# Performance work log

Hardware: AMD Instinct MI355X
Metric: run time of the kernel (lower is better)

## Reference

```python
import jax, jax.numpy as jnp
import numpy as np

NUM_GRAPHS = 4096
EPS = 1e-6

def _ln(x, g, b):
    mu = jnp.mean(x, axis=-1, keepdims=True)
    var = jnp.mean(jnp.square(x - mu), axis=-1, keepdims=True)
    return (x - mu) * jax.lax.rsqrt(var + EPS) * g + b

def setup_inputs() -> dict:
    key = jax.random.key(0)
    ks = jax.random.split(key, 8)
    N, D, H, DRUG = 262144, 128, 8, 128
    feat = jax.random.normal(ks[0], (N, D), dtype=jnp.float32)
    batch = jnp.sort(jax.random.randint(ks[1], (N,), 0, NUM_GRAPHS)).astype(jnp.int64)
    def lin(k, fi, fo):
        lim = 1.0 / np.sqrt(fi)
        return jax.random.uniform(k, (fi, fo), jnp.float32, -lim, lim)
    return {
        'feat': feat, 'batch': batch,
        'W1': lin(ks[2], D, 64), 'b1': jnp.zeros((64,), jnp.float32),
        'g1': jnp.ones((64,), jnp.float32), 'beta1': jnp.zeros((64,), jnp.float32),
        'W2': lin(ks[3], 64, H), 'b2': jnp.zeros((H,), jnp.float32),
        'W3': lin(ks[4], H * D, D), 'b3': jnp.zeros((D,), jnp.float32),
        'g3': jnp.ones((D,), jnp.float32), 'beta3': jnp.zeros((D,), jnp.float32),
        'W4': lin(ks[5], D, DRUG), 'b4': jnp.zeros((DRUG,), jnp.float32),
        'g4': jnp.ones((DRUG,), jnp.float32), 'beta4': jnp.zeros((DRUG,), jnp.float32),
    }

def reference(feat, batch, W1, b1, g1, beta1, W2, b2, W3, b3, g3, beta3, W4, b4, g4, beta4):
    seg = batch.astype(jnp.int32)
    # ATFC: Linear -> LeakyReLU -> LayerNorm -> Linear
    h = jax.nn.leaky_relu(feat @ W1 + b1)
    h = _ln(h, g1, beta1)
    att = jnp.exp(h @ W2 + b2)                      # [N, H]
    # segment softmax normalization
    s = jax.ops.segment_sum(att, seg, num_segments=NUM_GRAPHS)  # [B, H]
    att = att / s[seg]
    # weighted aggregation: outer product + segment sum -> [B, H, D]
    out = jax.ops.segment_sum(att[:, :, None] * feat[:, None, :], seg, num_segments=NUM_GRAPHS)
    out = out.reshape(NUM_GRAPHS, -1)               # [B, H*D]
    # output block (dropout is identity in eval mode)
    o = _ln(jax.nn.leaky_relu(out @ W3 + b3), g3, beta3)
    o = _ln(jax.nn.leaky_relu(o @ W4 + b4), g4, beta4)
    return o
```

## Files before the change

kernel.cpp:

```cpp
#include <hip/hip_runtime.h>
#include <math.h>

#define NG 4096
#define NN 262144
#define D 128
#define M1 64
#define NH 8
#define EPS 1e-6f

typedef __attribute__((ext_vector_type(8))) short short8;
typedef __attribute__((ext_vector_type(4))) float f32x4;

__device__ inline float leaky(float x) { return x > 0.f ? x : 0.01f * x; }

__device__ inline short f2bf(float f) {
  union { float f; unsigned u; } v; v.f = f;
  unsigned r = (v.u + 0x7fffu + ((v.u >> 16) & 1u)) >> 16;
  return (short)r;
}

__global__ void k0_offs(const int* __restrict__ batch, int* __restrict__ offs) {
  int i = blockIdx.x * 256 + threadIdx.x;
  if (i <= NG) {
    int lo = 0, hi = NN;
    while (lo < hi) {
      int mid = (lo + hi) >> 1;
      if (batch[mid] < i) lo = mid + 1; else hi = mid;
    }
    offs[i] = lo;
  }
}

__global__ __launch_bounds__(256) void k1_att(
    const float* __restrict__ feat, const float* __restrict__ W1,
    const float* __restrict__ b1, const float* __restrict__ g1,
    const float* __restrict__ beta1, const float* __restrict__ W2,
    const float* __restrict__ b2, float* __restrict__ att) {
  __shared__ short W1T[M1][D + 8];
  __shared__ short W2T[16][M1 + 8];
  __shared__ short hb[128][72];

  int t = threadIdx.x;
#pragma unroll
  for (int i = 0; i < 8; ++i) {
    int idx4 = t + 256 * i;
    int k = idx4 >> 4;
    int j = (idx4 & 15) * 4;
    float4 wv = *(const float4*)(W1 + k * M1 + j);
    W1T[j + 0][k] = f2bf(wv.x);
    W1T[j + 1][k] = f2bf(wv.y);
    W1T[j + 2][k] = f2bf(wv.z);
    W1T[j + 3][k] = f2bf(wv.w);
  }
#pragma unroll
  for (int i = 0; i < 4; ++i) {
    int e = t * 4 + i;
    int hh = e >> 6, j = e & 63;
    W2T[hh][j] = (hh < NH) ? f2bf(W2[j * NH + hh]) : (short)0;
  }
  __syncthreads();

  int w = t >> 6, l = t & 63;
  int lr = l & 15, lq = l >> 4;
  int nb = blockIdx.x * 128 + w * 32;

  short8 afr[2][4];
#pragma unroll
  for (int mt = 0; mt < 2; ++mt) {
    const float* rp = feat + (size_t)(nb + mt * 16 + lr) * D + lq * 8;
#pragma unroll
    for (int c = 0; c < 4; ++c) {
      float4 x0 = *(const float4*)(rp + c * 32);
      float4 x1 = *(const float4*)(rp + c * 32 + 4);
      short8 a;
      a[0] = f2bf(x0.x); a[1] = f2bf(x0.y); a[2] = f2bf(x0.z); a[3] = f2bf(x0.w);
      a[4] = f2bf(x1.x); a[5] = f2bf(x1.y); a[6] = f2bf(x1.z); a[7] = f2bf(x1.w);
      afr[mt][c] = a;
    }
  }

  f32x4 acc[2][4];
#pragma unroll
  for (int mt = 0; mt < 2; ++mt)
#pragma unroll
    for (int nt = 0; nt < 4; ++nt) acc[mt][nt] = (f32x4){0.f, 0.f, 0.f, 0.f};
#pragma unroll
  for (int c = 0; c < 4; ++c) {
#pragma unroll
    for (int nt = 0; nt < 4; ++nt) {
      short8 bfr = *(const short8*)&W1T[nt * 16 + lr][c * 32 + lq * 8];
      acc[0][nt] = __builtin_amdgcn_mfma_f32_16x16x32_bf16(afr[0][c], bfr, acc[0][nt], 0, 0, 0);
      acc[1][nt] = __builtin_amdgcn_mfma_f32_16x16x32_bf16(afr[1][c], bfr, acc[1][nt], 0, 0, 0);
    }
  }

  float b1v[4], g1v[4], btv[4];
#pragma unroll
  for (int nt = 0; nt < 4; ++nt) {
    b1v[nt] = b1[nt * 16 + lr];
    g1v[nt] = g1[nt * 16 + lr];
    btv[nt] = beta1[nt * 16 + lr];
  }
#pragma unroll
  for (int mt = 0; mt < 2; ++mt) {
#pragma unroll
    for (int r = 0; r < 4; ++r) {
      float x[4], s1 = 0.f, s2 = 0.f;
#pragma unroll
      for (int nt = 0; nt < 4; ++nt) {
        float xv = leaky(acc[mt][nt][r] + b1v[nt]);
        x[nt] = xv;
        s1 += xv;
        s2 = fmaf(xv, xv, s2);
      }
#pragma unroll
      for (int off = 1; off < 16; off <<= 1) {
        s1 += __shfl_xor(s1, off);
        s2 += __shfl_xor(s2, off);
      }
      float mu = s1 * (1.f / M1);
      float var = s2 * (1.f / M1) - mu * mu;
      float inv = rsqrtf(var + EPS);
      int node = w * 32 + mt * 16 + lq * 4 + r;
#pragma unroll
      for (int nt = 0; nt < 4; ++nt)
        hb[node][nt * 16 + lr] = f2bf((x[nt] - mu) * inv * g1v[nt] + btv[nt]);
    }
  }
  __syncthreads();

  f32x4 acc2[2];
  acc2[0] = (f32x4){0.f, 0.f, 0.f, 0.f};
  acc2[1] = (f32x4){0.f, 0.f, 0.f, 0.f};
#pragma unroll
  for (int c2 = 0; c2 < 2; ++c2) {
    short8 bfr2 = *(const short8*)&W2T[lr][c2 * 32 + lq * 8];
#pragma unroll
    for (int mt = 0; mt < 2; ++mt) {
      short8 af2 = *(const short8*)&hb[w * 32 + mt * 16 + lr][c2 * 32 + lq * 8];
      acc2[mt] = __builtin_amdgcn_mfma_f32_16x16x32_bf16(af2, bfr2, acc2[mt], 0, 0, 0);
    }
  }
  if (lr < NH) {
    float b2v = b2[lr];
#pragma unroll
    for (int mt = 0; mt < 2; ++mt)
#pragma unroll
      for (int r = 0; r < 4; ++r) {
        int node = nb + mt * 16 + lq * 4 + r;
        att[(size_t)node * NH + lr] = expf(acc2[mt][r] + b2v);
      }
  }
}

__global__ __launch_bounds__(256) void k2_agg(
    const float* __restrict__ feat, const int* __restrict__ offs,
    const float* __restrict__ att, float* __restrict__ out_row) {
  __shared__ float4 red[4][NH][32];
  __shared__ float reds[4][NH][32];

  int g = blockIdx.x, t = threadIdx.x;
  int d4 = t & 31, sub = t >> 5;
  int lo = offs[g], hi = offs[g + 1];

  float4 acc[NH];
  float sa[NH];
#pragma unroll
  for (int h = 0; h < NH; ++h) {
    acc[h] = make_float4(0.f, 0.f, 0.f, 0.f);
    sa[h] = 0.f;
  }

  const float4* fv = (const float4*)feat;
  const float4* av = (const float4*)att;
  int n = lo + sub;
  float4 fc, a0c, a1c;
  if (n < hi) {
    fc = fv[(size_t)n * 32 + d4];
    a0c = av[(size_t)n * 2];
    a1c = av[(size_t)n * 2 + 1];
  }
  while (n < hi) {
    int n2 = n + 8;
    float4 fn, a0n, a1n;
    if (n2 < hi) {
      fn = fv[(size_t)n2 * 32 + d4];
      a0n = av[(size_t)n2 * 2];
      a1n = av[(size_t)n2 * 2 + 1];
    }
    float ah[NH] = {a0c.x, a0c.y, a0c.z, a0c.w, a1c.x, a1c.y, a1c.z, a1c.w};
#pragma unroll
    for (int h = 0; h < NH; ++h) {
      acc[h].x = fmaf(ah[h], fc.x, acc[h].x);
      acc[h].y = fmaf(ah[h], fc.y, acc[h].y);
      acc[h].z = fmaf(ah[h], fc.z, acc[h].z);
      acc[h].w = fmaf(ah[h], fc.w, acc[h].w);
      sa[h] += ah[h];
    }
    fc = fn; a0c = a0n; a1c = a1n;
    n = n2;
  }

  if (sub >= 4) {
#pragma unroll
    for (int h = 0; h < NH; ++h) {
      red[sub - 4][h][d4] = acc[h];
      reds[sub - 4][h][d4] = sa[h];
    }
  }
  __syncthreads();
  if (sub < 4) {
#pragma unroll
    for (int h = 0; h < NH; ++h) {
      float4 r = red[sub][h][d4];
      acc[h].x += r.x; acc[h].y += r.y; acc[h].z += r.z; acc[h].w += r.w;
      sa[h] += reds[sub][h][d4];
    }
  }
  __syncthreads();
  if (sub >= 2 && sub < 4) {
#pragma unroll
    for (int h = 0; h < NH; ++h) {
      red[sub - 2][h][d4] = acc[h];
      reds[sub - 2][h][d4] = sa[h];
    }
  }
  __syncthreads();
  if (sub < 2) {
#pragma unroll
    for (int h = 0; h < NH; ++h) {
      float4 r = red[sub][h][d4];
      acc[h].x += r.x; acc[h].y += r.y; acc[h].z += r.z; acc[h].w += r.w;
      sa[h] += reds[sub][h][d4];
    }
  }
  __syncthreads();
  if (sub == 1) {
#pragma unroll
    for (int h = 0; h < NH; ++h) {
      red[0][h][d4] = acc[h];
      reds[0][h][d4] = sa[h];
    }
  }
  __syncthreads();
  if (sub == 0) {
    float4* orow = (float4*)(out_row + (size_t)g * (NH * D));
#pragma unroll
    for (int h = 0; h < NH; ++h) {
      float4 r = red[0][h][d4];
      float st = sa[h] + reds[0][h][d4];
      float inv = st > 0.f ? 1.f / st : 0.f;
      float4 v;
      v.x = (acc[h].x + r.x) * inv;
      v.y = (acc[h].y + r.y) * inv;
      v.z = (acc[h].z + r.z) * inv;
      v.w = (acc[h].w + r.w) * inv;
      orow[h * 32 + d4] = v;
    }
  }
}

__global__ __launch_bounds__(256) void k3_mlp(
    const float* __restrict__ out_row, const float* __restrict__ W3,
    const float* __restrict__ b3, const float* __restrict__ g3,
    const float* __restrict__ beta3, const float* __restrict__ W4,
    const float* __restrict__ b4, const float* __restrict__ g4,
    const float* __restrict__ beta4, float* __restrict__ out) {
  __shared__ float X[8][1024];
  __shared__ float p1[2][8][128];
  __shared__ float h2[8][128];
  __shared__ float o2[8][128];

  int gb = blockIdx.x * 8;
  int t = threadIdx.x;

  {
    const float4* src = (const float4*)(out_row + (size_t)gb * (NH * D));
    float4* dst = (float4*)&X[0][0];
#pragma unroll
    for (int i = 0; i < 8; ++i) dst[t + 256 * i] = src[t + 256 * i];
  }
  __syncthreads();

  int j2 = (t & 63) * 2, gq = ((t >> 6) & 1) * 4, half = t >> 7;
  float a[4][2];
#pragma unroll
  for (int i = 0; i < 4; ++i) { a[i][0] = 0.f; a[i][1] = 0.f; }
  int k0 = half * 512;
  for (int k = k0; k < k0 + 512; k += 4) {
    float4 xv[4];
#pragma unroll
    for (int i = 0; i < 4; ++i) xv[i] = *(const float4*)&X[gq + i][k];
#pragma unroll
    for (int kk = 0; kk < 4; ++kk) {
      float2 wv = *(const float2*)(W3 + (size_t)(k + kk) * D + j2);
#pragma unroll
      for (int i = 0; i < 4; ++i) {
        float x = (&xv[i].x)[kk];
        a[i][0] = fmaf(x, wv.x, a[i][0]);
        a[i][1] = fmaf(x, wv.y, a[i][1]);
      }
    }
  }
#pragma unroll
  for (int i = 0; i < 4; ++i)
    *(float2*)&p1[half][gq + i][j2] = make_float2(a[i][0], a[i][1]);
  __syncthreads();

  int g = t >> 5, c0 = (t & 31) * 4;
  {
    float v[4], sum = 0.f, sq = 0.f;
#pragma unroll
    for (int i = 0; i < 4; ++i) {
      float x = leaky(p1[0][g][c0 + i] + p1[1][g][c0 + i] + b3[c0 + i]);
      v[i] = x;
      sum += x;
      sq = fmaf(x, x, sq);
    }
#pragma unroll
    for (int off = 16; off > 0; off >>= 1) {
      sum += __shfl_xor(sum, off);
      sq += __shfl_xor(sq, off);
    }
    float mu = sum * (1.f / D);
    float var = sq * (1.f / D) - mu * mu;
    float inv = rsqrtf(var + EPS);
#pragma unroll
    for (int i = 0; i < 4; ++i)
      h2[g][c0 + i] = (v[i] - mu) * inv * g3[c0 + i] + beta3[c0 + i];
  }
  __syncthreads();

  {
    int j = t & 127, gh = (t >> 7) * 4;
    float a2[4] = {0.f, 0.f, 0.f, 0.f};
    for (int k = 0; k < 128; k += 4) {
      float4 hv[4];
#pragma unroll
      for (int i = 0; i < 4; ++i) hv[i] = *(const float4*)&h2[gh + i][k];
#pragma unroll
      for (int kk = 0; kk < 4; ++kk) {
        float wv = W4[(size_t)(k + kk) * D + j];
#pragma unroll
        for (int i = 0; i < 4; ++i) a2[i] = fmaf((&hv[i].x)[kk], wv, a2[i]);
      }
    }
#pragma unroll
    for (int i = 0; i < 4; ++i) o2[gh + i][j] = a2[i];
  }
  __syncthreads();

  {
    float v[4], sum = 0.f, sq = 0.f;
#pragma unroll
    for (int i = 0; i < 4; ++i) {
      float x = leaky(o2[g][c0 + i] + b4[c0 + i]);
      v[i] = x;
      sum += x;
      sq = fmaf(x, x, sq);
    }
#pragma unroll
    for (int off = 16; off > 0; off >>= 1) {
      sum += __shfl_xor(sum, off);
      sq += __shfl_xor(sq, off);
    }
    float mu = sum * (1.f / D);
    float var = sq * (1.f / D) - mu * mu;
    float inv = rsqrtf(var + EPS);
    float4 res;
#pragma unroll
    for (int i = 0; i < 4; ++i)
      (&res.x)[i] = (v[i] - mu) * inv * g4[c0 + i] + beta4[c0 + i];
    *(float4*)(out + (size_t)(gb + g) * D + c0) = res;
  }
}

extern "C" void kernel_launch(void* const* d_in, const int* in_sizes, int n_in,
                              void* d_out, int out_size, void* d_ws, size_t ws_size,
                              hipStream_t stream) {
  (void)in_sizes; (void)n_in; (void)out_size; (void)ws_size;
  const float* feat  = (const float*)d_in[0];
  const int*   batch = (const int*)d_in[1];
  const float* W1    = (const float*)d_in[2];
  const float* b1    = (const float*)d_in[3];
  const float* g1    = (const float*)d_in[4];
  const float* beta1 = (const float*)d_in[5];
  const float* W2    = (const float*)d_in[6];
  const float* b2    = (const float*)d_in[7];
  const float* W3    = (const float*)d_in[8];
  const float* b3    = (const float*)d_in[9];
  const float* g3    = (const float*)d_in[10];
  const float* beta3 = (const float*)d_in[11];
  const float* W4    = (const float*)d_in[12];
  const float* b4    = (const float*)d_in[13];
  const float* g4    = (const float*)d_in[14];
  const float* beta4 = (const float*)d_in[15];
  float* out = (float*)d_out;

  char* ws = (char*)d_ws;
  float* att     = (float*)ws;
  float* out_row = (float*)(ws + (size_t)NN * NH * 4);
  int*   offs    = (int*)(ws + (size_t)NN * NH * 4 + (size_t)NG * NH * D * 4);

  k0_offs<<<(NG + 256) / 256, 256, 0, stream>>>(batch, offs);
  k1_att<<<NN / 128, 256, 0, stream>>>(feat, W1, b1, g1, beta1, W2, b2, att);
  k2_agg<<<NG, 256, 0, stream>>>(feat, offs, att, out_row);
  k3_mlp<<<NG / 8, 256, 0, stream>>>(out_row, W3, b3, g3, beta3, W4, b4, g4,
                                     beta4, out);
}
```

Measured before the change: 301.4 us.

## Move output MLP to bf16 MFMA and use one wave per graph in aggregation

Adds a prep kernel that transposes W3 and W4 into bf16 column-major copies. The output MLP now runs both matmuls on bf16 MFMA with 16 graphs per 128-thread block, replacing the scalar fp32 FMA loops. The aggregation kernel now gives each graph a single wave with a two-slot prefetch and a shuffle reduction, removing the multi-stage shared-memory tree and its barriers. The trade-off is bf16 rounding in the final layers and less parallelism per graph in the aggregation.

```diff
diff --git a/kernel.cpp b/kernel.cpp
--- a/kernel.cpp
+++ b/kernel.cpp
@@ -29,6 +29,36 @@
     }
     offs[i] = lo;
   }
+}
+
+__global__ __launch_bounds__(256) void k0b_prep(
+    const float* __restrict__ W3, const float* __restrict__ W4,
+    short* __restrict__ W3T, short* __restrict__ W4T) {
+  __shared__ float tile[64][65];
+  int b = blockIdx.x, t = threadIdx.x;
+  const float* src; short* dst; int kt, nt, tkl;
+  if (b < 32) { src = W3; dst = W3T; kt = b >> 1; nt = b & 1; tkl = 1024; }
+  else        { src = W4; dst = W4T; kt = (b - 32) >> 1; nt = (b - 32) & 1; tkl = 128; }
+
+#pragma unroll
+  for (int i = 0; i < 4; ++i) {
+    int id = t + 256 * i;
+    int r = id >> 4, c4 = (id & 15) * 4;
+    float4 v = *(const float4*)(src + (size_t)(kt * 64 + r) * D + nt * 64 + c4);
+    tile[r][c4 + 0] = v.x; tile[r][c4 + 1] = v.y;
+    tile[r][c4 + 2] = v.z; tile[r][c4 + 3] = v.w;
+  }
+  __syncthreads();
+  int n = t >> 2, kb = (t & 3) * 16;
+  short8 p0, p1;
+#pragma unroll
+  for (int j = 0; j < 8; ++j) {
+    p0[j] = f2bf(tile[kb + j][n]);
+    p1[j] = f2bf(tile[kb + 8 + j][n]);
+  }
+  short* o = dst + (size_t)(nt * 64 + n) * tkl + kt * 64 + kb;
+  *(short8*)o = p0;
+  *(short8*)(o + 8) = p1;
 }
 
 __global__ __launch_bounds__(256) void k1_att(
@@ -156,11 +186,10 @@
 __global__ __launch_bounds__(256) void k2_agg(
     const float* __restrict__ feat, const int* __restrict__ offs,
     const float* __restrict__ att, float* __restrict__ out_row) {
-  __shared__ float4 red[4][NH][32];
-  __shared__ float reds[4][NH][32];
-
-  int g = blockIdx.x, t = threadIdx.x;
-  int d4 = t & 31, sub = t >> 5;
+  int t = threadIdx.x;
+  int w = t >> 6, l = t & 63;
+  int g = blockIdx.x * 4 + w;
+  int d4 = l & 31, sub = l >> 5;
   int lo = offs[g], hi = offs[g + 1];
 
   float4 acc[NH];
@@ -173,22 +202,31 @@
 
   const float4* fv = (const float4*)feat;
   const float4* av = (const float4*)att;
-  int n = lo + sub;
-  float4 fc, a0c, a1c;
-  if (n < hi) {
-    fc = fv[(size_t)n * 32 + d4];
-    a0c = av[(size_t)n * 2];
-    a1c = av[(size_t)n * 2 + 1];
-  }
-  while (n < hi) {
-    int n2 = n + 8;
+
+  float4 fb[2], a0b[2], a1b[2];
+  int n0 = lo + sub;
+#pragma unroll
+  for (int i = 0; i < 2; ++i) {
+    int ni = n0 + i * 2;
+    if (ni < hi) {
+      fb[i] = fv[(size_t)ni * 32 + d4];
+      a0b[i] = av[(size_t)ni * 2];
+      a1b[i] = av[(size_t)ni * 2 + 1];
+    }
+  }
+  int it = 0;
+  for (int n = n0; n < hi; n += 2, ++it) {
+    int slot = it & 1;
+    int np = n + 4;
     float4 fn, a0n, a1n;
-    if (n2 < hi) {
-      fn = fv[(size_t)n2 * 32 + d4];
-      a0n = av[(size_t)n2 * 2];
-      a1n = av[(size_t)n2 * 2 + 1];
-    }
-    float ah[NH] = {a0c.x, a0c.y, a0c.z, a0c.w, a1c.x, a1c.y, a1c.z, a1c.w};
+    bool pf = np < hi;
+    if (pf) {
+      fn = fv[(size_t)np * 32 + d4];
+      a0n = av[(size_t)np * 2];
+      a1n = av[(size_t)np * 2 + 1];
+    }
+    float4 fc = fb[slot], A0 = a0b[slot], A1 = a1b[slot];
+    float ah[NH] = {A0.x, A0.y, A0.z, A0.w, A1.x, A1.y, A1.z, A1.w};
 #pragma unroll
     for (int h = 0; h < NH; ++h) {
       acc[h].x = fmaf(ah[h], fc.x, acc[h].x);
@@ -197,181 +235,173 @@
       acc[h].w = fmaf(ah[h], fc.w, acc[h].w);
       sa[h] += ah[h];
     }
-    fc = fn; a0c = a0n; a1c = a1n;
-    n = n2;
-  }
-
-  if (sub >= 4) {
-#pragma unroll
-    for (int h = 0; h < NH; ++h) {
-      red[sub - 4][h][d4] = acc[h];
-      reds[sub - 4][h][d4] = sa[h];
-    }
-  }
-  __syncthreads();
-  if (sub < 4) {
-#pragma unroll
-    for (int h = 0; h < NH; ++h) {
-      float4 r = red[sub][h][d4];
-      acc[h].x += r.x; acc[h].y += r.y; acc[h].z += r.z; acc[h].w += r.w;
-      sa[h] += reds[sub][h][d4];
-    }
-  }
-  __syncthreads();
-  if (sub >= 2 && sub < 4) {
-#pragma unroll
-    for (int h = 0; h < NH; ++h) {
-      red[sub - 2][h][d4] = acc[h];
-      reds[sub - 2][h][d4] = sa[h];
-    }
-  }
-  __syncthreads();
-  if (sub < 2) {
-#pragma unroll
-    for (int h = 0; h < NH; ++h) {
-      float4 r = red[sub][h][d4];
-      acc[h].x += r.x; acc[h].y += r.y; acc[h].z += r.z; acc[h].w += r.w;
-      sa[h] += reds[sub][h][d4];
-    }
-  }
-  __syncthreads();
-  if (sub == 1) {
-#pragma unroll
-    for (int h = 0; h < NH; ++h) {
-      red[0][h][d4] = acc[h];
-      reds[0][h][d4] = sa[h];
-    }
-  }
-  __syncthreads();
+    if (pf) { fb[slot] = fn; a0b[slot] = a0n; a1b[slot] = a1n; }
+  }
+
+#pragma unroll
+  for (int h = 0; h < NH; ++h) {
+    acc[h].x += __shfl_xor(acc[h].x, 32);
+    acc[h].y += __shfl_xor(acc[h].y, 32);
+    acc[h].z += __shfl_xor(acc[h].z, 32);
+    acc[h].w += __shfl_xor(acc[h].w, 32);
+    sa[h] += __shfl_xor(sa[h], 32);
+  }
+
   if (sub == 0) {
     float4* orow = (float4*)(out_row + (size_t)g * (NH * D));
 #pragma unroll
     for (int h = 0; h < NH; ++h) {
-      float4 r = red[0][h][d4];
-      float st = sa[h] + reds[0][h][d4];
-      float inv = st > 0.f ? 1.f / st : 0.f;
+      float inv = (hi > lo) ? 1.f / sa[h] : 0.f;
       float4 v;
-      v.x = (acc[h].x + r.x) * inv;
-      v.y = (acc[h].y + r.y) * inv;
-      v.z = (acc[h].z + r.z) * inv;
-      v.w = (acc[h].w + r.w) * inv;
+      v.x = acc[h].x * inv; v.y = acc[h].y * inv;
+      v.z = acc[h].z * inv; v.w = acc[h].w * inv;
       orow[h * 32 + d4] = v;
     }
   }
 }
 
-__global__ __launch_bounds__(256) void k3_mlp(
-    const float* __restrict__ out_row, const float* __restrict__ W3,
+__global__ __launch_bounds__(128) void k3_mlp(
+    const float* __restrict__ X, const short* __restrict__ W3T,
     const float* __restrict__ b3, const float* __restrict__ g3,
-    const float* __restrict__ beta3, const float* __restrict__ W4,
+    const float* __restrict__ beta3, const short* __restrict__ W4T,
     const float* __restrict__ b4, const float* __restrict__ g4,
     const float* __restrict__ beta4, float* __restrict__ out) {
-  __shared__ float X[8][1024];
-  __shared__ float p1[2][8][128];
-  __shared__ float h2[8][128];
-  __shared__ float o2[8][128];
-
-  int gb = blockIdx.x * 8;
+  __shared__ short hbuf[16][136];
+  __shared__ float red[2][2][16];
+
   int t = threadIdx.x;
-
-  {
-    const float4* src = (const float4*)(out_row + (size_t)gb * (NH * D));
-    float4* dst = (float4*)&X[0][0];
-#pragma unroll
-    for (int i = 0; i < 8; ++i) dst[t + 256 * i] = src[t + 256 * i];
-  }
-  __syncthreads();
-
-  int j2 = (t & 63) * 2, gq = ((t >> 6) & 1) * 4, half = t >> 7;
-  float a[4][2];
-#pragma unroll
-  for (int i = 0; i < 4; ++i) { a[i][0] = 0.f; a[i][1] = 0.f; }
-  int k0 = half * 512;
-  for (int k = k0; k < k0 + 512; k += 4) {
-    float4 xv[4];
-#pragma unroll
-    for (int i = 0; i < 4; ++i) xv[i] = *(const float4*)&X[gq + i][k];
-#pragma unroll
-    for (int kk = 0; kk < 4; ++kk) {
-      float2 wv = *(const float2*)(W3 + (size_t)(k + kk) * D + j2);
-#pragma unroll
-      for (int i = 0; i < 4; ++i) {
-        float x = (&xv[i].x)[kk];
-        a[i][0] = fmaf(x, wv.x, a[i][0]);
-        a[i][1] = fmaf(x, wv.y, a[i][1]);
-      }
-    }
-  }
-#pragma unroll
-  for (int i = 0; i < 4; ++i)
-    *(float2*)&p1[half][gq + i][j2] = make_float2(a[i][0], a[i][1]);
-  __syncthreads();
-
-  int g = t >> 5, c0 = (t & 31) * 4;
-  {
-    float v[4], sum = 0.f, sq = 0.f;
-#pragma unroll
-    for (int i = 0; i < 4; ++i) {
-      float x = leaky(p1[0][g][c0 + i] + p1[1][g][c0 + i] + b3[c0 + i]);
-      v[i] = x;
-      sum += x;
-      sq = fmaf(x, x, sq);
-    }
-#pragma unroll
-    for (int off = 16; off > 0; off >>= 1) {
-      sum += __shfl_xor(sum, off);
-      sq += __shfl_xor(sq, off);
-    }
-    float mu = sum * (1.f / D);
-    float var = sq * (1.f / D) - mu * mu;
-    float inv = rsqrtf(var + EPS);
-#pragma unroll
-    for (int i = 0; i < 4; ++i)
-      h2[g][c0 + i] = (v[i] - mu) * inv * g3[c0 + i] + beta3[c0 + i];
-  }
-  __syncthreads();
-
-  {
-    int j = t & 127, gh = (t >> 7) * 4;
-    float a2[4] = {0.f, 0.f, 0.f, 0.f};
-    for (int k = 0; k < 128; k += 4) {
-      float4 hv[4];
-#pragma unroll
-      for (int i = 0; i < 4; ++i) hv[i] = *(const float4*)&h2[gh + i][k];
-#pragma unroll
-      for (int kk = 0; kk < 4; ++kk) {
-        float wv = W4[(size_t)(k + kk) * D + j];
-#pragma unroll
-        for (int i = 0; i < 4; ++i) a2[i] = fmaf((&hv[i].x)[kk], wv, a2[i]);
-      }
-    }
-#pragma unroll
-    for (int i = 0; i < 4; ++i) o2[gh + i][j] = a2[i];
-  }
-  __syncthreads();
-
-  {
-    float v[4], sum = 0.f, sq = 0.f;
-#pragma unroll
-    for (int i = 0; i < 4; ++i) {
-      float x = leaky(o2[g][c0 + i] + b4[c0 + i]);
-      v[i] = x;
-      sum += x;
-      sq = fmaf(x, x, sq);
-    }
-#pragma unroll
-    for (int off = 16; off > 0; off >>= 1) {
-      sum += __shfl_xor(sum, off);
-      sq += __shfl_xor(sq, off);
-    }
-    float mu = sum * (1.f / D);
-    float var = sq * (1.f / D) - mu * mu;
-    float inv = rsqrtf(var + EPS);
-    float4 res;
-#pragma unroll
-    for (int i = 0; i < 4; ++i)
-      (&res.x)[i] = (v[i] - mu) * inv * g4[c0 + i] + beta4[c0 + i];
-    *(float4*)(out + (size_t)(gb + g) * D + c0) = res;
+  int nw = t >> 6, l = t & 63;
+  int lr = l & 15, lq = l >> 4;
+  int gb = blockIdx.x * 16;
+
+  const float* xrow = X + (size_t)(gb + lr) * (NH * D) + lq * 8;
+  f32x4 acc[4];
+#pragma unroll
+  for (int nt = 0; nt < 4; ++nt) acc[nt] = (f32x4){0.f, 0.f, 0.f, 0.f};
+
+  float4 x0 = *(const float4*)(xrow);
+  float4 x1 = *(const float4*)(xrow + 4);
+  for (int kc = 0; kc < 32; ++kc) {
+    float4 nx0, nx1;
+    if (kc < 31) {
+      nx0 = *(const float4*)(xrow + (kc + 1) * 32);
+      nx1 = *(const float4*)(xrow + (kc + 1) * 32 + 4);
+    }
+    short8 a;
+    a[0] = f2bf(x0.x); a[1] = f2bf(x0.y); a[2] = f2bf(x0.z); a[3] = f2bf(x0.w);
+    a[4] = f2bf(x1.x); a[5] = f2bf(x1.y); a[6] = f2bf(x1.z); a[7] = f2bf(x1.w);
+#pragma unroll
+    for (int nt = 0; nt < 4; ++nt) {
+      int ncol = nw * 64 + nt * 16 + lr;
+      short8 b = *(const short8*)(W3T + (size_t)ncol * 1024 + kc * 32 + lq * 8);
+      acc[nt] = __builtin_amdgcn_mfma_f32_16x16x32_bf16(a, b, acc[nt], 0, 0, 0);
+    }
+    x0 = nx0; x1 = nx1;
+  }
+
+  float xv[4][4], s1[4] = {0.f, 0.f, 0.f, 0.f}, s2[4] = {0.f, 0.f, 0.f, 0.f};
+#pragma unroll
+  for (int nt = 0; nt < 4; ++nt) {
+    float bb = b3[nw * 64 + nt * 16 + lr];
+#pragma unroll
+    for (int r = 0; r < 4; ++r) {
+      float v = leaky(acc[nt][r] + bb);
+      xv[nt][r] = v;
+      s1[r] += v;
+      s2[r] = fmaf(v, v, s2[r]);
+    }
+  }
+#pragma unroll
+  for (int off = 1; off < 16; off <<= 1) {
+#pragma unroll
+    for (int r = 0; r < 4; ++r) {
+      s1[r] += __shfl_xor(s1[r], off);
+      s2[r] += __shfl_xor(s2[r], off);
+    }
+  }
+  if (lr == 0) {
+#pragma unroll
+    for (int r = 0; r < 4; ++r) {
+      red[nw][0][lq * 4 + r] = s1[r];
+      red[nw][1][lq * 4 + r] = s2[r];
+    }
+  }
+  __syncthreads();
+#pragma unroll
+  for (int nt = 0; nt < 4; ++nt) {
+    int col = nw * 64 + nt * 16 + lr;
+    float gg = g3[col], bt = beta3[col];
+#pragma unroll
+    for (int r = 0; r < 4; ++r) {
+      int row = lq * 4 + r;
+      float S1 = red[0][0][row] + red[1][0][row];
+      float S2 = red[0][1][row] + red[1][1][row];
+      float mu = S1 * (1.f / D);
+      float var = S2 * (1.f / D) - mu * mu;
+      float inv = rsqrtf(var + EPS);
+      hbuf[row][col] = f2bf((xv[nt][r] - mu) * inv * gg + bt);
+    }
+  }
+  __syncthreads();
+
+  f32x4 acc2[4];
+#pragma unroll
+  for (int nt = 0; nt < 4; ++nt) acc2[nt] = (f32x4){0.f, 0.f, 0.f, 0.f};
+#pragma unroll
+  for (int kc = 0; kc < 4; ++kc) {
+    short8 a2 = *(const short8*)&hbuf[lr][kc * 32 + lq * 8];
+#pragma unroll
+    for (int nt = 0; nt < 4; ++nt) {
+      int ncol = nw * 64 + nt * 16 + lr;
+      short8 b2 = *(const short8*)(W4T + (size_t)ncol * 128 + kc * 32 + lq * 8);
+      acc2[nt] = __builtin_amdgcn_mfma_f32_16x16x32_bf16(a2, b2, acc2[nt], 0, 0, 0);
+    }
+  }
+
+#pragma unroll
+  for (int r = 0; r < 4; ++r) { s1[r] = 0.f; s2[r] = 0.f; }
+#pragma unroll
+  for (int nt = 0; nt < 4; ++nt) {
+    float bb = b4[nw * 64 + nt * 16 + lr];
+#pragma unroll
+    for (int r = 0; r < 4; ++r) {
+      float v = leaky(acc2[nt][r] + bb);
+      xv[nt][r] = v;
+      s1[r] += v;
+      s2[r] = fmaf(v, v, s2[r]);
+    }
+  }
+#pragma unroll
+  for (int off = 1; off < 16; off <<= 1) {
+#pragma unroll
+    for (int r = 0; r < 4; ++r) {
+      s1[r] += __shfl_xor(s1[r], off);
+      s2[r] += __shfl_xor(s2[r], off);
+    }
+  }
+  __syncthreads();
+  if (lr == 0) {
+#pragma unroll
+    for (int r = 0; r < 4; ++r) {
+      red[nw][0][lq * 4 + r] = s1[r];
+      red[nw][1][lq * 4 + r] = s2[r];
+    }
+  }
+  __syncthreads();
+#pragma unroll
+  for (int nt = 0; nt < 4; ++nt) {
+    int col = nw * 64 + nt * 16 + lr;
+    float gg = g4[col], bt = beta4[col];
+#pragma unroll
+    for (int r = 0; r < 4; ++r) {
+      int row = lq * 4 + r;
+      float S1 = red[0][0][row] + red[1][0][row];
+      float S2 = red[0][1][row] + red[1][1][row];
+      float mu = S1 * (1.f / D);
+      float var = S2 * (1.f / D) - mu * mu;
+      float inv = rsqrtf(var + EPS);
+      out[(size_t)(gb + row) * D + col] = (xv[nt][r] - mu) * inv * gg + bt;
+    }
   }
 }
 
@@ -400,11 +430,15 @@
   char* ws = (char*)d_ws;
   float* att     = (float*)ws;
   float* out_row = (float*)(ws + (size_t)NN * NH * 4);
-  int*   offs    = (int*)(ws + (size_t)NN * NH * 4 + (size_t)NG * NH * D * 4);
+  char*  p       = ws + (size_t)NN * NH * 4 + (size_t)NG * NH * D * 4;
+  int*   offs    = (int*)p;
+  short* W3T     = (short*)(p + 32768);
+  short* W4T     = (short*)(p + 32768 + 262144);
 
   k0_offs<<<(NG + 256) / 256, 256, 0, stream>>>(batch, offs);
+  k0b_prep<<<36, 256, 0, stream>>>(W3, W4, W3T, W4T);
   k1_att<<<NN / 128, 256, 0, stream>>>(feat, W1, b1, g1, beta1, W2, b2, att);
-  k2_agg<<<NG, 256, 0, stream>>>(feat, offs, att, out_row);
-  k3_mlp<<<NG / 8, 256, 0, stream>>>(out_row, W3, b3, g3, beta3, W4, b4, g4,
-                                     beta4, out);
-}
+  k2_agg<<<NG / 4, 256, 0, stream>>>(feat, offs, att, out_row);
+  k3_mlp<<<NG / 16, 128, 0, stream>>>(out_row, W3T, b3, g3, beta3, W4T, b4, g4,
+                                      beta4, out);
+}
```

Result: slower. 327.9 us (+8.8%).
